# Optimization experiments

Hardware: AMD Instinct MI355X
Metric: run time of the kernel (lower is better)

The kernel has to match this reference:

```python
import jax, jax.numpy as jnp
import numpy as np

TEMPERATURE = 8.0  # sqrt(d_k) with d_k = 64

def setup_inputs() -> dict:
    key = jax.random.key(0)
    kq, kk, kv = jax.random.split(key, 3)
    B, L, D = 16, 2048, 64  # heads, seq_len, head_dim
    q = jax.random.normal(kq, (B, L, D), dtype=jnp.float32)
    k = jax.random.normal(kk, (B, L, D), dtype=jnp.float32)
    v = jax.random.normal(kv, (B, L, D), dtype=jnp.float32)
    return {"q": q, "k": k, "v": v}

def reference(q, k, v):
    # scores: [B, Lq, Lk]
    scores = jnp.einsum('bqd,bkd->bqk', q, k) / TEMPERATURE
    log_attn = jax.nn.log_softmax(scores, axis=-1)
    attn = jnp.exp(log_attn)  # softmax, reusing the single stable reduction
    out = jnp.einsum('bqk,bkd->bqd', attn, v)        # [B, Lq, Dv]
    B, Lk, Dv = v.shape
    # transpose(0,1).reshape(Lk, Dv*B): heads folded into feature dim
    output = jnp.transpose(out, (1, 0, 2)).reshape(Lk, Dv * B)
    return (output, attn, log_attn)
```

## Files before the change

kernel.cpp:

```cpp
#include <hip/hip_runtime.h>

#define LSEQ 2048
#define NH   16
#define HD   64

typedef __attribute__((ext_vector_type(8))) short short8;
typedef __attribute__((ext_vector_type(4))) float f32x4;

__device__ __forceinline__ unsigned short f2b(float x) {
  unsigned int u = __builtin_bit_cast(unsigned int, x);
  u += 0x7FFFu + ((u >> 16) & 1u);
  return (unsigned short)(u >> 16);
}

__global__ __launch_bounds__(256) void prep_kernel(
    const float* __restrict__ q, const float* __restrict__ k, const float* __restrict__ v,
    unsigned short* __restrict__ qb, unsigned short* __restrict__ kb,
    unsigned short* __restrict__ vt) {
  const int b = blockIdx.y, lt = blockIdx.x;
  const int t = threadIdx.x;
  __shared__ float vlds[64][65];
  const int l0 = lt * 64;
  #pragma unroll
  for (int i = 0; i < 4; ++i) {
    int r = (t >> 4) + 16 * i;
    size_t base = ((size_t)(b * LSEQ + l0 + r)) * HD + (t & 15) * 4;
    float4 qv = *(const float4*)(q + base);
    float4 kv = *(const float4*)(k + base);
    float4 vv = *(const float4*)(v + base);
    ushort4 qo, ko;
    qo.x = f2b(qv.x * 0.125f); qo.y = f2b(qv.y * 0.125f);
    qo.z = f2b(qv.z * 0.125f); qo.w = f2b(qv.w * 0.125f);
    ko.x = f2b(kv.x); ko.y = f2b(kv.y); ko.z = f2b(kv.z); ko.w = f2b(kv.w);
    *(ushort4*)(qb + base) = qo;
    *(ushort4*)(kb + base) = ko;
    int c = (t & 15) * 4;
    vlds[r][c] = vv.x; vlds[r][c + 1] = vv.y; vlds[r][c + 2] = vv.z; vlds[r][c + 3] = vv.w;
  }
  __syncthreads();
  const int ll = t & 63;
  const int dbase = (t >> 6) * 16;
  #pragma unroll
  for (int i = 0; i < 16; ++i) {
    int d = dbase + i;
    vt[((size_t)(b * HD + d)) * LSEQ + l0 + ll] = f2b(vlds[ll][d]);
  }
}

__global__ __launch_bounds__(256) void attn_kernel(
    const unsigned short* __restrict__ qb, const unsigned short* __restrict__ kb,
    const unsigned short* __restrict__ vt,
    float* __restrict__ out0, float* __restrict__ attn, float* __restrict__ logp) {
  const int b = blockIdx.y, qt = blockIdx.x;
  const int t = threadIdx.x;
  const int w = t >> 6, lane = t & 63, quad = lane >> 4, l16 = lane & 15;
  __shared__ unsigned short ps[4][16][72];

  const int q0 = qt * 64;
  const int qrl = quad * 4;

  const unsigned short* qrow = qb + ((size_t)(b * LSEQ + q0 + w * 16 + l16)) * HD;
  short8 aq0 = *(const short8*)(qrow + quad * 8);
  short8 aq1 = *(const short8*)(qrow + 32 + quad * 8);

  float p0 = 0.f, p1 = 0.f, p2 = 0.f, p3 = 0.f;
  for (int kt = 0; kt < 32; ++kt) {
    const unsigned short* kbase = kb + ((size_t)(b * LSEQ + kt * 64)) * HD;
    #pragma unroll
    for (int nt = 0; nt < 4; ++nt) {
      const unsigned short* krow = kbase + (nt * 16 + l16) * HD + quad * 8;
      short8 b0 = *(const short8*)(krow);
      short8 b1 = *(const short8*)(krow + 32);
      f32x4 s = {0.f, 0.f, 0.f, 0.f};
      s = __builtin_amdgcn_mfma_f32_16x16x32_bf16(aq0, b0, s, 0, 0, 0);
      s = __builtin_amdgcn_mfma_f32_16x16x32_bf16(aq1, b1, s, 0, 0, 0);
      p0 += __expf(s[0]); p1 += __expf(s[1]);
      p2 += __expf(s[2]); p3 += __expf(s[3]);
    }
  }
  #pragma unroll
  for (int off = 1; off < 16; off <<= 1) {
    p0 += __shfl_xor(p0, off, 64);
    p1 += __shfl_xor(p1, off, 64);
    p2 += __shfl_xor(p2, off, 64);
    p3 += __shfl_xor(p3, off, 64);
  }
  const float logl0 = __logf(p0), logl1 = __logf(p1);
  const float logl2 = __logf(p2), logl3 = __logf(p3);

  f32x4 oacc[4] = {{0.f,0.f,0.f,0.f},{0.f,0.f,0.f,0.f},{0.f,0.f,0.f,0.f},{0.f,0.f,0.f,0.f}};
  const size_t arow0 = ((size_t)(b * LSEQ + q0 + w * 16 + qrl)) * LSEQ;

  for (int kt = 0; kt < 32; ++kt) {
    const unsigned short* kbase = kb + ((size_t)(b * LSEQ + kt * 64)) * HD;
    #pragma unroll
    for (int nt = 0; nt < 4; ++nt) {
      const unsigned short* krow = kbase + (nt * 16 + l16) * HD + quad * 8;
      short8 b0 = *(const short8*)(krow);
      short8 b1 = *(const short8*)(krow + 32);
      f32x4 s = {0.f, 0.f, 0.f, 0.f};
      s = __builtin_amdgcn_mfma_f32_16x16x32_bf16(aq0, b0, s, 0, 0, 0);
      s = __builtin_amdgcn_mfma_f32_16x16x32_bf16(aq1, b1, s, 0, 0, 0);
      const int col = kt * 64 + nt * 16 + l16;
      const float la0 = s[0] - logl0; const float a0 = __expf(la0);
      const float la1 = s[1] - logl1; const float a1 = __expf(la1);
      const float la2 = s[2] - logl2; const float a2 = __expf(la2);
      const float la3 = s[3] - logl3; const float a3 = __expf(la3);
      attn[arow0 + col]            = a0;  logp[arow0 + col]            = la0;
      attn[arow0 + LSEQ + col]     = a1;  logp[arow0 + LSEQ + col]     = la1;
      attn[arow0 + 2 * LSEQ + col] = a2;  logp[arow0 + 2 * LSEQ + col] = la2;
      attn[arow0 + 3 * LSEQ + col] = a3;  logp[arow0 + 3 * LSEQ + col] = la3;
      ps[w][qrl + 0][nt * 16 + l16] = f2b(a0);
      ps[w][qrl + 1][nt * 16 + l16] = f2b(a1);
      ps[w][qrl + 2][nt * 16 + l16] = f2b(a2);
      ps[w][qrl + 3][nt * 16 + l16] = f2b(a3);
    }
    asm volatile("s_waitcnt lgkmcnt(0)" ::: "memory");
    short8 ap0 = *(const short8*)(&ps[w][l16][quad * 8]);
    short8 ap1 = *(const short8*)(&ps[w][l16][32 + quad * 8]);
    #pragma unroll
    for (int nt = 0; nt < 4; ++nt) {
      const unsigned short* vrow =
          vt + ((size_t)(b * HD + nt * 16 + l16)) * LSEQ + kt * 64 + quad * 8;
      short8 v0 = *(const short8*)(vrow);
      short8 v1 = *(const short8*)(vrow + 32);
      oacc[nt] = __builtin_amdgcn_mfma_f32_16x16x32_bf16(ap0, v0, oacc[nt], 0, 0, 0);
      oacc[nt] = __builtin_amdgcn_mfma_f32_16x16x32_bf16(ap1, v1, oacc[nt], 0, 0, 0);
    }
    asm volatile("s_waitcnt lgkmcnt(0)" ::: "memory");
  }

  #pragma unroll
  for (int nt = 0; nt < 4; ++nt) {
    #pragma unroll
    for (int r = 0; r < 4; ++r) {
      out0[((size_t)(q0 + w * 16 + qrl + r)) * (NH * HD) + b * HD + nt * 16 + l16] =
          oacc[nt][r];
    }
  }
}

extern "C" void kernel_launch(void* const* d_in, const int* in_sizes, int n_in,
                              void* d_out, int out_size, void* d_ws, size_t ws_size,
                              hipStream_t stream) {
  const float* q = (const float*)d_in[0];
  const float* k = (const float*)d_in[1];
  const float* v = (const float*)d_in[2];
  float* out0 = (float*)d_out;
  float* attn = out0 + (size_t)LSEQ * NH * HD;
  float* logp = attn + (size_t)NH * LSEQ * LSEQ;

  unsigned short* qb = (unsigned short*)d_ws;
  unsigned short* kb = qb + (size_t)NH * LSEQ * HD;
  unsigned short* vt = kb + (size_t)NH * LSEQ * HD;

  dim3 grid(LSEQ / 64, NH);
  prep_kernel<<<grid, 256, 0, stream>>>(q, k, v, qb, kb, vt);
  attn_kernel<<<grid, 256, 0, stream>>>(qb, kb, vt, out0, attn, logp);
}
```

Measured before the change: 702.3 us.

## Pre-swizzle Q/K/V into MFMA fragment order for fully coalesced loads

The prep kernel now writes Q, K and V in bf16 laid out in the exact per-lane fragment order the 16x16x32 MFMA consumes, staging tiles in LDS to do the reordering. The attention kernel then loads each operand fragment as one contiguous short8 per lane, so a wavefront reads 1KB contiguously instead of strided row segments. This is meant to cut memory transactions on the K and V operand loads in both passes. The cost is more LDS use and transpose work in the prep kernel. The attention kernel is probably bound by the large fp32 attn/logp writes, which this does not change.

```diff
diff --git a/kernel.cpp b/kernel.cpp
--- a/kernel.cpp
+++ b/kernel.cpp
@@ -15,41 +15,62 @@
 
 __global__ __launch_bounds__(256) void prep_kernel(
     const float* __restrict__ q, const float* __restrict__ k, const float* __restrict__ v,
-    unsigned short* __restrict__ qb, unsigned short* __restrict__ kb,
-    unsigned short* __restrict__ vt) {
+    unsigned short* __restrict__ qf, unsigned short* __restrict__ kf,
+    unsigned short* __restrict__ vf) {
   const int b = blockIdx.y, lt = blockIdx.x;
   const int t = threadIdx.x;
-  __shared__ float vlds[64][65];
+  __shared__ unsigned short qls[64][80];
+  __shared__ unsigned short kls[64][80];
+  __shared__ float vls[64][65];
   const int l0 = lt * 64;
+
   #pragma unroll
-  for (int i = 0; i < 4; ++i) {
-    int r = (t >> 4) + 16 * i;
-    size_t base = ((size_t)(b * LSEQ + l0 + r)) * HD + (t & 15) * 4;
-    float4 qv = *(const float4*)(q + base);
-    float4 kv = *(const float4*)(k + base);
-    float4 vv = *(const float4*)(v + base);
-    ushort4 qo, ko;
-    qo.x = f2b(qv.x * 0.125f); qo.y = f2b(qv.y * 0.125f);
-    qo.z = f2b(qv.z * 0.125f); qo.w = f2b(qv.w * 0.125f);
-    ko.x = f2b(kv.x); ko.y = f2b(kv.y); ko.z = f2b(kv.z); ko.w = f2b(kv.w);
-    *(ushort4*)(qb + base) = qo;
-    *(ushort4*)(kb + base) = ko;
-    int c = (t & 15) * 4;
-    vlds[r][c] = vv.x; vlds[r][c + 1] = vv.y; vlds[r][c + 2] = vv.z; vlds[r][c + 3] = vv.w;
+  for (int i = 0; i < 2; ++i) {
+    int c = t + i * 256;
+    int r = c >> 3, d0 = (c & 7) * 8;
+    size_t base = ((size_t)(b * LSEQ + l0 + r)) * HD + d0;
+    float4 qa = *(const float4*)(q + base);
+    float4 qc = *(const float4*)(q + base + 4);
+    float4 ka = *(const float4*)(k + base);
+    float4 kc = *(const float4*)(k + base + 4);
+    float4 va = *(const float4*)(v + base);
+    float4 vc = *(const float4*)(v + base + 4);
+    qls[r][d0 + 0] = f2b(qa.x * 0.125f); qls[r][d0 + 1] = f2b(qa.y * 0.125f);
+    qls[r][d0 + 2] = f2b(qa.z * 0.125f); qls[r][d0 + 3] = f2b(qa.w * 0.125f);
+    qls[r][d0 + 4] = f2b(qc.x * 0.125f); qls[r][d0 + 5] = f2b(qc.y * 0.125f);
+    qls[r][d0 + 6] = f2b(qc.z * 0.125f); qls[r][d0 + 7] = f2b(qc.w * 0.125f);
+    kls[r][d0 + 0] = f2b(ka.x); kls[r][d0 + 1] = f2b(ka.y);
+    kls[r][d0 + 2] = f2b(ka.z); kls[r][d0 + 3] = f2b(ka.w);
+    kls[r][d0 + 4] = f2b(kc.x); kls[r][d0 + 5] = f2b(kc.y);
+    kls[r][d0 + 6] = f2b(kc.z); kls[r][d0 + 7] = f2b(kc.w);
+    vls[r][d0 + 0] = va.x; vls[r][d0 + 1] = va.y;
+    vls[r][d0 + 2] = va.z; vls[r][d0 + 3] = va.w;
+    vls[r][d0 + 4] = vc.x; vls[r][d0 + 5] = vc.y;
+    vls[r][d0 + 6] = vc.z; vls[r][d0 + 7] = vc.w;
   }
   __syncthreads();
-  const int ll = t & 63;
-  const int dbase = (t >> 6) * 16;
+
   #pragma unroll
-  for (int i = 0; i < 16; ++i) {
-    int d = dbase + i;
-    vt[((size_t)(b * HD + d)) * LSEQ + l0 + ll] = f2b(vlds[ll][d]);
+  for (int i = 0; i < 2; ++i) {
+    int c = t + i * 256;
+    int l16 = c & 15, quad = (c >> 4) & 3, kk = (c >> 6) & 1, bl4 = c >> 7;
+    short8 qv = *(const short8*)(&qls[bl4 * 16 + l16][kk * 32 + quad * 8]);
+    short8 kv = *(const short8*)(&kls[bl4 * 16 + l16][kk * 32 + quad * 8]);
+    size_t dst = ((((size_t)b * 128 + lt * 4 + bl4) * 2 + kk) * 64 + quad * 16 + l16) * 8;
+    *(short8*)(qf + dst) = qv;
+    *(short8*)(kf + dst) = kv;
+    short8 vv8;
+    #pragma unroll
+    for (int j = 0; j < 8; ++j)
+      vv8[j] = (short)f2b(vls[kk * 32 + quad * 8 + j][bl4 * 16 + l16]);
+    size_t dstv = ((((size_t)b * 32 + lt) * 8 + bl4 * 2 + kk) * 64 + quad * 16 + l16) * 8;
+    *(short8*)(vf + dstv) = vv8;
   }
 }
 
 __global__ __launch_bounds__(256) void attn_kernel(
-    const unsigned short* __restrict__ qb, const unsigned short* __restrict__ kb,
-    const unsigned short* __restrict__ vt,
+    const unsigned short* __restrict__ qf, const unsigned short* __restrict__ kf,
+    const unsigned short* __restrict__ vf,
     float* __restrict__ out0, float* __restrict__ attn, float* __restrict__ logp) {
   const int b = blockIdx.y, qt = blockIdx.x;
   const int t = threadIdx.x;
@@ -59,18 +80,20 @@
   const int q0 = qt * 64;
   const int qrl = quad * 4;
 
-  const unsigned short* qrow = qb + ((size_t)(b * LSEQ + q0 + w * 16 + l16)) * HD;
-  short8 aq0 = *(const short8*)(qrow + quad * 8);
-  short8 aq1 = *(const short8*)(qrow + 32 + quad * 8);
+  const size_t qbase = (((size_t)b * 128 + qt * 4 + w) * 2 * 64 + lane) * 8;
+  short8 aq0 = *(const short8*)(qf + qbase);
+  short8 aq1 = *(const short8*)(qf + qbase + 512);
+
+  const unsigned short* kfb = kf + (size_t)b * 128 * 2 * 64 * 8;
+  const unsigned short* vfb = vf + (size_t)b * 32 * 8 * 64 * 8;
 
   float p0 = 0.f, p1 = 0.f, p2 = 0.f, p3 = 0.f;
   for (int kt = 0; kt < 32; ++kt) {
-    const unsigned short* kbase = kb + ((size_t)(b * LSEQ + kt * 64)) * HD;
     #pragma unroll
     for (int nt = 0; nt < 4; ++nt) {
-      const unsigned short* krow = kbase + (nt * 16 + l16) * HD + quad * 8;
-      short8 b0 = *(const short8*)(krow);
-      short8 b1 = *(const short8*)(krow + 32);
+      const unsigned short* kp = kfb + ((size_t)(kt * 4 + nt) * 128 + lane) * 8;
+      short8 b0 = *(const short8*)(kp);
+      short8 b1 = *(const short8*)(kp + 512);
       f32x4 s = {0.f, 0.f, 0.f, 0.f};
       s = __builtin_amdgcn_mfma_f32_16x16x32_bf16(aq0, b0, s, 0, 0, 0);
       s = __builtin_amdgcn_mfma_f32_16x16x32_bf16(aq1, b1, s, 0, 0, 0);
@@ -92,12 +115,11 @@
   const size_t arow0 = ((size_t)(b * LSEQ + q0 + w * 16 + qrl)) * LSEQ;
 
   for (int kt = 0; kt < 32; ++kt) {
-    const unsigned short* kbase = kb + ((size_t)(b * LSEQ + kt * 64)) * HD;
     #pragma unroll
     for (int nt = 0; nt < 4; ++nt) {
-      const unsigned short* krow = kbase + (nt * 16 + l16) * HD + quad * 8;
-      short8 b0 = *(const short8*)(krow);
-      short8 b1 = *(const short8*)(krow + 32);
+      const unsigned short* kp = kfb + ((size_t)(kt * 4 + nt) * 128 + lane) * 8;
+      short8 b0 = *(const short8*)(kp);
+      short8 b1 = *(const short8*)(kp + 512);
       f32x4 s = {0.f, 0.f, 0.f, 0.f};
       s = __builtin_amdgcn_mfma_f32_16x16x32_bf16(aq0, b0, s, 0, 0, 0);
       s = __builtin_amdgcn_mfma_f32_16x16x32_bf16(aq1, b1, s, 0, 0, 0);
@@ -120,10 +142,9 @@
     short8 ap1 = *(const short8*)(&ps[w][l16][32 + quad * 8]);
     #pragma unroll
     for (int nt = 0; nt < 4; ++nt) {
-      const unsigned short* vrow =
-          vt + ((size_t)(b * HD + nt * 16 + l16)) * LSEQ + kt * 64 + quad * 8;
-      short8 v0 = *(const short8*)(vrow);
-      short8 v1 = *(const short8*)(vrow + 32);
+      const unsigned short* vp = vfb + ((size_t)(kt * 8 + nt * 2) * 64 + lane) * 8;
+      short8 v0 = *(const short8*)(vp);
+      short8 v1 = *(const short8*)(vp + 512);
       oacc[nt] = __builtin_amdgcn_mfma_f32_16x16x32_bf16(ap0, v0, oacc[nt], 0, 0, 0);
       oacc[nt] = __builtin_amdgcn_mfma_f32_16x16x32_bf16(ap1, v1, oacc[nt], 0, 0, 0);
     }
@@ -150,11 +171,11 @@
   float* attn = out0 + (size_t)LSEQ * NH * HD;
   float* logp = attn + (size_t)NH * LSEQ * LSEQ;
 
-  unsigned short* qb = (unsigned short*)d_ws;
-  unsigned short* kb = qb + (size_t)NH * LSEQ * HD;
-  unsigned short* vt = kb + (size_t)NH * LSEQ * HD;
+  unsigned short* qf = (unsigned short*)d_ws;
+  unsigned short* kf = qf + (size_t)NH * LSEQ * HD;
+  unsigned short* vf = kf + (size_t)NH * LSEQ * HD;
 
   dim3 grid(LSEQ / 64, NH);
-  prep_kernel<<<grid, 256, 0, stream>>>(q, k, v, qb, kb, vt);
-  attn_kernel<<<grid, 256, 0, stream>>>(qb, kb, vt, out0, attn, logp);
+  prep_kernel<<<grid, 256, 0, stream>>>(q, k, v, qf, kf, vf);
+  attn_kernel<<<grid, 256, 0, stream>>>(qf, kf, vf, out0, attn, logp);
 }
```

After: 642.5 us. -8.5%, faster.
